# Kernel tuning notes

Measured on AMD Instinct MI355X. Metric: run time of the kernel, lower is better.

## Reference

```python
import jax, jax.numpy as jnp
import numpy as np

DIM = 2048
N_HEADS = 32
N_KV_HEADS = 8
HEAD_DIM = DIM // N_HEADS  # 64
SEQ = 2048
BATCH = 2


def _rope_freqs(seq_len, head_dim, theta=10000.0):
    inv = 1.0 / (theta ** (np.arange(0, head_dim, 2)[: head_dim // 2].astype(np.float32) / head_dim))
    t = np.arange(seq_len, dtype=np.float32)
    ang = np.outer(t, inv)  # (seq, head_dim//2)
    return jnp.asarray(np.cos(ang)), jnp.asarray(np.sin(ang))


def setup_inputs() -> dict:
    key = jax.random.key(0)
    ks = jax.random.split(key, 5)
    x = jax.random.normal(ks[0], (BATCH, SEQ, DIM), dtype=jnp.float32)
    s = 1.0 / np.sqrt(DIM)
    wq = jax.random.normal(ks[1], (N_HEADS * HEAD_DIM, DIM), dtype=jnp.float32) * s
    wk = jax.random.normal(ks[2], (N_KV_HEADS * HEAD_DIM, DIM), dtype=jnp.float32) * s
    wv = jax.random.normal(ks[3], (N_KV_HEADS * HEAD_DIM, DIM), dtype=jnp.float32) * s
    wo = jax.random.normal(ks[4], (DIM, N_HEADS * HEAD_DIM), dtype=jnp.float32) * s
    freqs_cos, freqs_sin = _rope_freqs(SEQ, HEAD_DIM)
    return {"x": x, "freqs_cos": freqs_cos, "freqs_sin": freqs_sin,
            "wq": wq, "wk": wk, "wv": wv, "wo": wo}


def _apply_rope(t, cos, sin):
    # t: (B, S, H, D); cos/sin: (S, D//2) broadcast to (1, S, 1, D//2)
    B, S, H, D = t.shape
    tr = t.reshape(B, S, H, D // 2, 2)
    x0, x1 = tr[..., 0], tr[..., 1]
    c = cos[None, :, None, :]
    s = sin[None, :, None, :]
    o0 = x0 * c - x1 * s
    o1 = x0 * s + x1 * c
    return jnp.stack([o0, o1], axis=-1).reshape(B, S, H, D)


def reference(x, freqs_cos, freqs_sin, wq, wk, wv, wo):
    B, S, _ = x.shape
    H, KV, D = N_HEADS, N_KV_HEADS, HEAD_DIM
    rep = H // KV
    xq = jnp.einsum('bsd,hd->bsh', x, wq).reshape(B, S, H, D)
    xk = jnp.einsum('bsd,hd->bsh', x, wk).reshape(B, S, KV, D)
    xv = jnp.einsum('bsd,hd->bsh', x, wv).reshape(B, S, KV, D)
    xq = _apply_rope(xq, freqs_cos, freqs_sin)
    xk = _apply_rope(xk, freqs_cos, freqs_sin)
    # GQA without materializing repeated K/V: group q heads as (KV, rep).
    # repeat_interleave on dim=2 maps q head h -> kv head h // rep.
    xqg = xq.reshape(B, S, KV, rep, D)
    scale = 1.0 / jnp.sqrt(jnp.float32(D))
    scores = jnp.einsum('bqkrd,bskd->bkrqs', xqg, xk) * scale  # (B,KV,rep,S,S)
    causal = jnp.tril(jnp.ones((S, S), dtype=bool))
    scores = jnp.where(causal[None, None, None], scores, jnp.float32(-jnp.inf))
    probs = jax.nn.softmax(scores, axis=-1)
    out = jnp.einsum('bkrqs,bskd->bqkrd', probs, xv)  # (B,S,KV,rep,D)
    out = out.reshape(B, S, H * D)
    return jnp.einsum('bsh,dh->bsd', out, wo)
```

## Files before the change

kernel.cpp:

```cpp
#include <hip/hip_runtime.h>

#define DIMSZ 2048
#define NH 32
#define NKV 8
#define HD 64
#define SEQLEN 2048
#define BATCH 2
#define NROWS (BATCH*SEQLEN)
#define NQKVC 3072

typedef __bf16 bf16x8 __attribute__((ext_vector_type(8)));
typedef __bf16 bf16x2 __attribute__((ext_vector_type(2)));
typedef float f32x4v __attribute__((ext_vector_type(4)));
typedef float f32x2v __attribute__((ext_vector_type(2)));
typedef float f32x16 __attribute__((ext_vector_type(16)));

__device__ __forceinline__ unsigned short f2bf(float f) {
  __bf16 h = (__bf16)f;
  union { __bf16 h; unsigned short u; } v; v.h = h; return v.u;
}
__device__ __forceinline__ unsigned int pk2bf(float lo, float hi) {
  f32x2v v; v[0] = lo; v[1] = hi;
  bf16x2 h = __builtin_convertvector(v, bf16x2);
  union { bf16x2 h; unsigned int u; } c; c.h = h; return c.u;
}
__device__ __forceinline__ int swz128(int row, int colBytes) {
  return row * 128 + (colBytes ^ ((row & 7) << 4));
}

#define GLOAD16(g, l) __builtin_amdgcn_global_load_lds( \
    (const __attribute__((address_space(1))) unsigned int*)(g), \
    (__attribute__((address_space(3))) unsigned int*)(l), 16, 0, 0)

__global__ void k_cvt_all(const float* __restrict__ x,
                          const float* __restrict__ wq, const float* __restrict__ wk,
                          const float* __restrict__ wv, const float* __restrict__ wo,
                          unsigned short* __restrict__ xb,
                          unsigned short* __restrict__ wqkvb,
                          unsigned short* __restrict__ wob) {
  int i = blockIdx.x * 256 + threadIdx.x;
  const float* s; unsigned short* d; int soff, doff;
  if (i < 2097152)        { s = x;  d = xb;    soff = i;           doff = i; }
  else if (i < 3145728)   { s = wq; d = wqkvb; soff = i - 2097152; doff = i - 2097152; }
  else if (i < 3407872)   { s = wk; d = wqkvb; soff = i - 3145728; doff = i - 2097152; }
  else if (i < 3670016)   { s = wv; d = wqkvb; soff = i - 3407872; doff = i - 2097152; }
  else                    { s = wo; d = wob;   soff = i - 3670016; doff = i - 3670016; }
  float4 v = reinterpret_cast<const float4*>(s)[soff];
  uint2 pk; pk.x = pk2bf(v.x, v.y); pk.y = pk2bf(v.z, v.w);
  reinterpret_cast<uint2*>(d)[doff] = pk;
}

__global__ __launch_bounds__(256, 2) void k_gemm_qkv(
    const unsigned short* __restrict__ A,
    const unsigned short* __restrict__ B,
    const float* __restrict__ fc, const float* __restrict__ fs,
    unsigned short* __restrict__ Qb, unsigned short* __restrict__ Kb,
    unsigned short* __restrict__ Vt)
{
  constexpr int BK = 64, K = DIMSZ;
  __shared__ __attribute__((aligned(16))) unsigned short smA[128 * BK];
  __shared__ __attribute__((aligned(16))) unsigned short smB[128 * BK];
  const int tid = threadIdx.x;
  const int lane = tid & 63;
  const int wid = tid >> 6;
  const int lr = lane & 15, lg = lane >> 4;
  const int gx = gridDim.x;
  int lin = blockIdx.y * gx + blockIdx.x;
  const int cpx = (gx * gridDim.y) >> 3;
  lin = (lin & 7) * cpx + (lin >> 3);
  const int m0 = (lin / gx) * 128, n0 = (lin % gx) * 128;
  const int wr = (wid >> 1) * 64, wc = (wid & 1) * 64;

  f32x4v acc[4][4];
  #pragma unroll
  for (int i = 0; i < 4; i++)
    #pragma unroll
    for (int j = 0; j < 4; j++)
      acc[i][j] = f32x4v{0.f, 0.f, 0.f, 0.f};

  for (int k0 = 0; k0 < K; k0 += BK) {
    #pragma unroll
    for (int c = 0; c < 4; c++) {
      const int chunk = wid * 4 + c;
      const int idx = chunk * 64 + lane;
      const int row = idx >> 3, s = idx & 7;
      const int ks = (s ^ (row & 7)) * 8;
      GLOAD16(A + (size_t)(m0 + row) * K + k0 + ks, &smA[chunk * 512]);
      GLOAD16(B + (size_t)(n0 + row) * K + k0 + ks, &smB[chunk * 512]);
    }
    __syncthreads();
    #pragma unroll
    for (int ks = 0; ks < 2; ks++) {
      bf16x8 af[4], bfv[4];
      #pragma unroll
      for (int m = 0; m < 4; m++)
        af[m] = *reinterpret_cast<const bf16x8*>((char*)smA + swz128(wr + m * 16 + lr, ks * 64 + lg * 16));
      #pragma unroll
      for (int n = 0; n < 4; n++)
        bfv[n] = *reinterpret_cast<const bf16x8*>((char*)smB + swz128(wc + n * 16 + lr, ks * 64 + lg * 16));
      #pragma unroll
      for (int m = 0; m < 4; m++)
        #pragma unroll
        for (int n = 0; n < 4; n++)
          acc[m][n] = __builtin_amdgcn_mfma_f32_16x16x32_bf16(af[m], bfv[n], acc[m][n], 0, 0, 0);
    }
    __syncthreads();
  }
  const int bx = n0 >> 7;
  if (bx < 20) {
    const bool isQ = bx < 16;
    const float SCL = isQ ? 0.18033688011112043f : 1.0f;
    #pragma unroll
    for (int n = 0; n < 4; n++) {
      const int col = n0 + wc + n * 16 + lr;
      const int d = col & 63;
      const int i = d >> 1;
      const float sgn = (d & 1) ? 1.0f : -1.0f;
      unsigned short* dst;
      if (isQ) dst = Qb + (size_t)(col >> 6) * (SEQLEN * HD) + d;
      else     dst = Kb + (size_t)((col - 2048) >> 6) * (SEQLEN * HD) + d;
      #pragma unroll
      for (int m = 0; m < 4; m++)
        #pragma unroll
        for (int r = 0; r < 4; r++) {
          const int row = m0 + wr + m * 16 + lg * 4 + r;
          const int s = row & (SEQLEN - 1), b = row >> 11;
          const float v = acc[m][n][r];
          const float p = __shfl_xor(v, 1);
          const float c = fc[s * 32 + i], sn = fs[s * 32 + i];
          const float o = (v * c + sgn * p * sn) * SCL;
          const size_t headStride = (size_t)(isQ ? NH : NKV) * SEQLEN * HD;
          dst[(size_t)b * headStride + (size_t)s * HD] = f2bf(o);
        }
    }
  } else {
    #pragma unroll
    for (int n = 0; n < 4; n++) {
      const int col = n0 + wc + n * 16 + lr;
      const int kvh = (col - 2560) >> 6, d = col & 63;
      #pragma unroll
      for (int m = 0; m < 4; m++) {
        const int row0 = m0 + wr + m * 16 + lg * 4;
        const int s0 = row0 & (SEQLEN - 1), b = row0 >> 11;
        uint2 pk;
        pk.x = pk2bf(acc[m][n][0], acc[m][n][1]);
        pk.y = pk2bf(acc[m][n][2], acc[m][n][3]);
        *reinterpret_cast<uint2*>(
            Vt + ((size_t)((b * NKV + kvh) * HD) + d) * SEQLEN + s0) = pk;
      }
    }
  }
}

template<int OUT_BF16>
__global__ __launch_bounds__(256, 2) void k_gemm_bt(
    const unsigned short* __restrict__ A,
    const unsigned short* __restrict__ B,
    void* __restrict__ Cv, int M, int N, int K)
{
  constexpr int BK = 64;
  __shared__ __attribute__((aligned(16))) unsigned short smA[128 * BK];
  __shared__ __attribute__((aligned(16))) unsigned short smB[128 * BK];
  const int tid = threadIdx.x;
  const int lane = tid & 63;
  const int wid = tid >> 6;
  const int lr = lane & 15, lg = lane >> 4;
  const int gx = gridDim.x;
  int lin = blockIdx.y * gx + blockIdx.x;
  const int cpx = (gx * gridDim.y) >> 3;
  lin = (lin & 7) * cpx + (lin >> 3);
  const int m0 = (lin / gx) * 128, n0 = (lin % gx) * 128;
  const int wr = (wid >> 1) * 64, wc = (wid & 1) * 64;

  f32x4v acc[4][4];
  #pragma unroll
  for (int i = 0; i < 4; i++)
    #pragma unroll
    for (int j = 0; j < 4; j++)
      acc[i][j] = f32x4v{0.f, 0.f, 0.f, 0.f};

  for (int k0 = 0; k0 < K; k0 += BK) {
    #pragma unroll
    for (int c = 0; c < 4; c++) {
      const int chunk = wid * 4 + c;
      const int idx = chunk * 64 + lane;
      const int row = idx >> 3, s = idx & 7;
      const int ks = (s ^ (row & 7)) * 8;
      GLOAD16(A + (size_t)(m0 + row) * K + k0 + ks, &smA[chunk * 512]);
      GLOAD16(B + (size_t)(n0 + row) * K + k0 + ks, &smB[chunk * 512]);
    }
    __syncthreads();
    #pragma unroll
    for (int ks = 0; ks < 2; ks++) {
      bf16x8 af[4], bfv[4];
      #pragma unroll
      for (int m = 0; m < 4; m++)
        af[m] = *reinterpret_cast<const bf16x8*>((char*)smA + swz128(wr + m * 16 + lr, ks * 64 + lg * 16));
      #pragma unroll
      for (int n = 0; n < 4; n++)
        bfv[n] = *reinterpret_cast<const bf16x8*>((char*)smB + swz128(wc + n * 16 + lr, ks * 64 + lg * 16));
      #pragma unroll
      for (int m = 0; m < 4; m++)
        #pragma unroll
        for (int n = 0; n < 4; n++)
          acc[m][n] = __builtin_amdgcn_mfma_f32_16x16x32_bf16(af[m], bfv[n], acc[m][n], 0, 0, 0);
    }
    __syncthreads();
  }
  #pragma unroll
  for (int m = 0; m < 4; m++)
    #pragma unroll
    for (int n = 0; n < 4; n++)
      #pragma unroll
      for (int r = 0; r < 4; r++) {
        const size_t row = m0 + wr + m * 16 + lg * 4 + r;
        const size_t col = n0 + wc + n * 16 + lr;
        if (OUT_BF16) ((unsigned short*)Cv)[row * N + col] = f2bf(acc[m][n][r]);
        else          ((float*)Cv)[row * N + col] = acc[m][n][r];
      }
}

__global__ __launch_bounds__(256, 2) void k_attn(
    const unsigned short* __restrict__ Qg,
    const unsigned short* __restrict__ Kg,
    const unsigned short* __restrict__ Vt,
    unsigned short* __restrict__ Og)
{
  constexpr int KVB = 64;
  __shared__ __attribute__((aligned(16))) unsigned short sK0[KVB * HD];
  __shared__ __attribute__((aligned(16))) unsigned short sK1[KVB * HD];
  __shared__ __attribute__((aligned(16))) unsigned short sV0[HD * KVB];
  __shared__ __attribute__((aligned(16))) unsigned short sV1[HD * KVB];
  const int tid = threadIdx.x;
  const int lane = tid & 63, wid = tid >> 6;
  const int l31 = lane & 31, hi = lane >> 5;
  const int g = blockIdx.x;
  const int i = g >> 3;
  const int r = i >> 5;
  const int c = i & 31;
  const int p = (g & 7) * 2 + (c >> 4);
  const int kvh = p & 7, b = p >> 3;
  const int h = kvh * 4 + r;
  const int s4 = c & 15;
  const int qt = (r & 1) ? s4 : 15 - s4;
  const unsigned short* Qp = Qg + ((size_t)(b * NH + h) * SEQLEN) * HD;
  const unsigned short* Kp = Kg + ((size_t)(b * NKV + kvh) * SEQLEN) * HD;
  const unsigned short* Vp = Vt + ((size_t)(b * NKV + kvh) * HD) * SEQLEN;

  int srow[2], scol[2];
  #pragma unroll
  for (int cc = 0; cc < 2; cc++) {
    const int idx = (wid * 2 + cc) * 64 + lane;
    srow[cc] = idx >> 3;
    scol[cc] = ((idx & 7) ^ (srow[cc] & 7)) * 8;
  }

  const int qrow0 = qt * 128 + wid * 32;
  const int qg = qrow0 + l31;
  bf16x8 aq[4];
  #pragma unroll
  for (int ks = 0; ks < 4; ks++)
    aq[ks] = *reinterpret_cast<const bf16x8*>(Qp + (size_t)qg * HD + ks * 16 + hi * 8);

  f32x16 accO0, accO1;
  #pragma unroll
  for (int ii = 0; ii < 16; ii++) { accO0[ii] = 0.f; accO1[ii] = 0.f; }
  float mrun = -3.0e38f, lrun = 0.f;

  auto compute = [&](int kv0, auto& sKb, auto& sVb) {
    if (kv0 > qrow0 + 31) return;
    f32x16 S0, S1;
    #pragma unroll
    for (int ii = 0; ii < 16; ii++) { S0[ii] = 0.f; S1[ii] = 0.f; }
    __builtin_amdgcn_s_setprio(1);
    #pragma unroll
    for (int ks = 0; ks < 4; ks++) {
      bf16x8 ak0 = *reinterpret_cast<const bf16x8*>((char*)sKb + swz128(l31,      ks * 32 + hi * 16));
      bf16x8 ak1 = *reinterpret_cast<const bf16x8*>((char*)sKb + swz128(32 + l31, ks * 32 + hi * 16));
      S0 = __builtin_amdgcn_mfma_f32_32x32x16_bf16(ak0, aq[ks], S0, 0, 0, 0);
      S1 = __builtin_amdgcn_mfma_f32_32x32x16_bf16(ak1, aq[ks], S1, 0, 0, 0);
    }
    __builtin_amdgcn_s_setprio(0);
    if (kv0 + KVB - 1 > qrow0) {
      #pragma unroll
      for (int reg = 0; reg < 16; reg++) {
        const int rl = (reg & 3) + 8 * (reg >> 2) + (hi << 2);
        if (kv0 + rl > qg)      S0[reg] = -1.0e30f;
        if (kv0 + 32 + rl > qg) S1[reg] = -1.0e30f;
      }
    }
    float t16[16];
    #pragma unroll
    for (int ii = 0; ii < 16; ii++) t16[ii] = fmaxf(S0[ii], S1[ii]);
    float t8[8];
    #pragma unroll
    for (int ii = 0; ii < 8; ii++) t8[ii] = fmaxf(t16[ii], t16[ii + 8]);
    float t4[4];
    #pragma unroll
    for (int ii = 0; ii < 4; ii++) t4[ii] = fmaxf(t8[ii], t8[ii + 4]);
    float tm = fmaxf(fmaxf(t4[0], t4[1]), fmaxf(t4[2], t4[3]));
    tm = fmaxf(tm, __shfl_xor(tm, 32));
    const float mo = mrun;
    const bool defer = __all(tm <= mo + 8.0f);
    const float mn = defer ? mo : fmaxf(mo, tm);
    #pragma unroll
    for (int ii = 0; ii < 16; ii++) {
      S0[ii] = __builtin_amdgcn_exp2f(S0[ii] - mn);
      S1[ii] = __builtin_amdgcn_exp2f(S1[ii] - mn);
    }
    float u16[16];
    #pragma unroll
    for (int ii = 0; ii < 16; ii++) u16[ii] = S0[ii] + S1[ii];
    float u8[8];
    #pragma unroll
    for (int ii = 0; ii < 8; ii++) u8[ii] = u16[ii] + u16[ii + 8];
    float u4[4];
    #pragma unroll
    for (int ii = 0; ii < 4; ii++) u4[ii] = u8[ii] + u8[ii + 4];
    float rs = (u4[0] + u4[1]) + (u4[2] + u4[3]);
    rs += __shfl_xor(rs, 32);
    if (defer) {
      lrun += rs;
    } else {
      const float sc = __builtin_amdgcn_exp2f(mo - mn);
      mrun = mn;
      lrun = lrun * sc + rs;
      #pragma unroll
      for (int reg = 0; reg < 16; reg++) {
        const int rl = (reg & 3) + 8 * (reg >> 2) + (hi << 2);
        const float scr = __shfl(sc, rl);
        accO0[reg] *= scr; accO1[reg] *= scr;
      }
    }
    __builtin_amdgcn_s_setprio(1);
    #define PVSTEP(S16, G, CB) do {                                          \
      unsigned a0 = pk2bf(S16[(G)+0], S16[(G)+1]);                           \
      unsigned a1 = pk2bf(S16[(G)+2], S16[(G)+3]);                           \
      unsigned b0 = pk2bf(S16[(G)+4], S16[(G)+5]);                           \
      unsigned b1 = pk2bf(S16[(G)+6], S16[(G)+7]);                           \
      unsigned s0 = hi ? a0 : b0, s1 = hi ? a1 : b1;                         \
      unsigned r0 = __shfl_xor((int)s0, 32), r1 = __shfl_xor((int)s1, 32);   \
      union { unsigned u[4]; bf16x8 v; } pf;                                 \
      pf.u[0] = hi ? r0 : a0; pf.u[1] = hi ? r1 : a1;                        \
      pf.u[2] = hi ? b0 : r0; pf.u[3] = hi ? b1 : r1;                        \
      bf16x8 bv0 = *reinterpret_cast<const bf16x8*>((char*)sVb + swz128(l31,      (CB))); \
      bf16x8 bv1 = *reinterpret_cast<const bf16x8*>((char*)sVb + swz128(32 + l31, (CB))); \
      accO0 = __builtin_amdgcn_mfma_f32_32x32x16_bf16(pf.v, bv0, accO0, 0, 0, 0); \
      accO1 = __builtin_amdgcn_mfma_f32_32x32x16_bf16(pf.v, bv1, accO1, 0, 0, 0); \
    } while (0)
    PVSTEP(S0, 0,  0  + hi * 16);
    PVSTEP(S0, 8,  32 + hi * 16);
    PVSTEP(S1, 0,  64 + hi * 16);
    PVSTEP(S1, 8,  96 + hi * 16);
    #undef PVSTEP
    __builtin_amdgcn_s_setprio(0);
  };

  const int nt = qt * 2 + 2;
  GLOAD16(Kp + (size_t)srow[0] * HD + scol[0], &sK0[(wid * 2 + 0) * 512]);
  GLOAD16(Kp + (size_t)srow[1] * HD + scol[1], &sK0[(wid * 2 + 1) * 512]);
  GLOAD16(Vp + (size_t)srow[0] * SEQLEN + scol[0], &sV0[(wid * 2 + 0) * 512]);
  GLOAD16(Vp + (size_t)srow[1] * SEQLEN + scol[1], &sV0[(wid * 2 + 1) * 512]);
  __syncthreads();
  for (int t = 0; t < nt; t += 2) {
    {
      const int kn = (t + 1) * KVB;
      GLOAD16(Kp + (size_t)(kn + srow[0]) * HD + scol[0], &sK1[(wid * 2 + 0) * 512]);
      GLOAD16(Kp + (size_t)(kn + srow[1]) * HD + scol[1], &sK1[(wid * 2 + 1) * 512]);
      GLOAD16(Vp + (size_t)srow[0] * SEQLEN + kn + scol[0], &sV1[(wid * 2 + 0) * 512]);
      GLOAD16(Vp + (size_t)srow[1] * SEQLEN + kn + scol[1], &sV1[(wid * 2 + 1) * 512]);
    }
    compute(t * KVB, sK0, sV0);
    __syncthreads();
    if (t + 2 < nt) {
      const int kn = (t + 2) * KVB;
      GLOAD16(Kp + (size_t)(kn + srow[0]) * HD + scol[0], &sK0[(wid * 2 + 0) * 512]);
      GLOAD16(Kp + (size_t)(kn + srow[1]) * HD + scol[1], &sK0[(wid * 2 + 1) * 512]);
      GLOAD16(Vp + (size_t)srow[0] * SEQLEN + kn + scol[0], &sV0[(wid * 2 + 0) * 512]);
      GLOAD16(Vp + (size_t)srow[1] * SEQLEN + kn + scol[1], &sV0[(wid * 2 + 1) * 512]);
    }
    compute((t + 1) * KVB, sK1, sV1);
    __syncthreads();
  }
  const float inv = 1.0f / lrun;
  #pragma unroll
  for (int reg = 0; reg < 16; reg++) {
    const int rl = (reg & 3) + 8 * (reg >> 2) + (hi << 2);
    const float invr = __shfl(inv, rl);
    const int q = qrow0 + rl;
    const size_t base = ((size_t)(b * SEQLEN + q)) * DIMSZ + h * HD;
    Og[base + l31]      = f2bf(accO0[reg] * invr);
    Og[base + 32 + l31] = f2bf(accO1[reg] * invr);
  }
}

extern "C" void kernel_launch(void* const* d_in, const int* in_sizes, int n_in,
                              void* d_out, int out_size, void* d_ws, size_t ws_size,
                              hipStream_t stream)
{
  const float* x  = (const float*)d_in[0];
  const float* fc = (const float*)d_in[1];
  const float* fs = (const float*)d_in[2];
  const float* wq = (const float*)d_in[3];
  const float* wk = (const float*)d_in[4];
  const float* wv = (const float*)d_in[5];
  const float* wo = (const float*)d_in[6];
  float* out = (float*)d_out;
  char* ws = (char*)d_ws;

  unsigned short* xb    = (unsigned short*)(ws + 0);
  unsigned short* wqkvb = (unsigned short*)(ws + 16777216);
  unsigned short* wob   = (unsigned short*)(ws + 29360128);
  unsigned short* Qb    = (unsigned short*)(ws + 62914560);
  unsigned short* Kb    = (unsigned short*)(ws + 79691776);
  unsigned short* Vtb   = (unsigned short*)(ws + 83886080);
  unsigned short* attnb = (unsigned short*)(ws + 88080384);

  k_cvt_all<<<18432, 256, 0, stream>>>(x, wq, wk, wv, wo, xb, wqkvb, wob);

  dim3 g1(24, 32);
  k_gemm_qkv<<<g1, 256, 0, stream>>>(xb, wqkvb, fc, fs, Qb, Kb, Vtb);

  k_attn<<<1024, 256, 0, stream>>>(Qb, Kb, Vtb, attnb);

  dim3 g2(16, 32);
  k_gemm_bt<0><<<g2, 256, 0, stream>>>(attnb, wob, out, NROWS, DIMSZ, DIMSZ);
}
```

Measured before the change: 188.9 us.

## Double attention query tile to 256 rows with 8 waves per block

The attention kernel now launches 512 blocks of 512 threads, each covering 256 query rows (8 waves of 32 rows) instead of 128 rows with 4 waves. Each K/V tile loaded into shared memory is reused by twice as many query rows, and each thread issues one cooperative load instead of two, which cuts global/L2 traffic per query row. Block scheduling changes from an interleaved/mirrored qt order to a longest-first descending order. In exchange, fewer and larger blocks may worsen load balance across the causal triangle, early waves idle on fully masked tiles, and launch_bounds(512,2) tightens the register budget.

```diff
diff --git a/kernel.cpp b/kernel.cpp
--- a/kernel.cpp
+++ b/kernel.cpp
@@ -220,7 +220,7 @@
       }
 }
 
-__global__ __launch_bounds__(256, 2) void k_attn(
+__global__ __launch_bounds__(512, 2) void k_attn(
     const unsigned short* __restrict__ Qg,
     const unsigned short* __restrict__ Kg,
     const unsigned short* __restrict__ Vt,
@@ -235,27 +235,21 @@
   const int lane = tid & 63, wid = tid >> 6;
   const int l31 = lane & 31, hi = lane >> 5;
   const int g = blockIdx.x;
-  const int i = g >> 3;
-  const int r = i >> 5;
-  const int c = i & 31;
-  const int p = (g & 7) * 2 + (c >> 4);
+  const int c = g >> 3;
+  const int qt = 7 - (c >> 3);
+  const int rem = c & 7;
+  const int p = (g & 7) * 2 + (rem >> 2);
   const int kvh = p & 7, b = p >> 3;
-  const int h = kvh * 4 + r;
-  const int s4 = c & 15;
-  const int qt = (r & 1) ? s4 : 15 - s4;
+  const int h = kvh * 4 + (rem & 3);
   const unsigned short* Qp = Qg + ((size_t)(b * NH + h) * SEQLEN) * HD;
   const unsigned short* Kp = Kg + ((size_t)(b * NKV + kvh) * SEQLEN) * HD;
   const unsigned short* Vp = Vt + ((size_t)(b * NKV + kvh) * HD) * SEQLEN;
 
-  int srow[2], scol[2];
-  #pragma unroll
-  for (int cc = 0; cc < 2; cc++) {
-    const int idx = (wid * 2 + cc) * 64 + lane;
-    srow[cc] = idx >> 3;
-    scol[cc] = ((idx & 7) ^ (srow[cc] & 7)) * 8;
-  }
-
-  const int qrow0 = qt * 128 + wid * 32;
+  const int sidx = wid * 64 + lane;
+  const int srow = sidx >> 3;
+  const int scol = ((sidx & 7) ^ (srow & 7)) * 8;
+
+  const int qrow0 = qt * 256 + wid * 32;
   const int qg = qrow0 + l31;
   bf16x8 aq[4];
   #pragma unroll
@@ -356,28 +350,22 @@
     __builtin_amdgcn_s_setprio(0);
   };
 
-  const int nt = qt * 2 + 2;
-  GLOAD16(Kp + (size_t)srow[0] * HD + scol[0], &sK0[(wid * 2 + 0) * 512]);
-  GLOAD16(Kp + (size_t)srow[1] * HD + scol[1], &sK0[(wid * 2 + 1) * 512]);
-  GLOAD16(Vp + (size_t)srow[0] * SEQLEN + scol[0], &sV0[(wid * 2 + 0) * 512]);
-  GLOAD16(Vp + (size_t)srow[1] * SEQLEN + scol[1], &sV0[(wid * 2 + 1) * 512]);
+  const int nt = (qt + 1) * 4;
+  GLOAD16(Kp + (size_t)srow * HD + scol, &sK0[wid * 512]);
+  GLOAD16(Vp + (size_t)srow * SEQLEN + scol, &sV0[wid * 512]);
   __syncthreads();
   for (int t = 0; t < nt; t += 2) {
     {
       const int kn = (t + 1) * KVB;
-      GLOAD16(Kp + (size_t)(kn + srow[0]) * HD + scol[0], &sK1[(wid * 2 + 0) * 512]);
-      GLOAD16(Kp + (size_t)(kn + srow[1]) * HD + scol[1], &sK1[(wid * 2 + 1) * 512]);
-      GLOAD16(Vp + (size_t)srow[0] * SEQLEN + kn + scol[0], &sV1[(wid * 2 + 0) * 512]);
-      GLOAD16(Vp + (size_t)srow[1] * SEQLEN + kn + scol[1], &sV1[(wid * 2 + 1) * 512]);
+      GLOAD16(Kp + (size_t)(kn + srow) * HD + scol, &sK1[wid * 512]);
+      GLOAD16(Vp + (size_t)srow * SEQLEN + kn + scol, &sV1[wid * 512]);
     }
     compute(t * KVB, sK0, sV0);
     __syncthreads();
     if (t + 2 < nt) {
       const int kn = (t + 2) * KVB;
-      GLOAD16(Kp + (size_t)(kn + srow[0]) * HD + scol[0], &sK0[(wid * 2 + 0) * 512]);
-      GLOAD16(Kp + (size_t)(kn + srow[1]) * HD + scol[1], &sK0[(wid * 2 + 1) * 512]);
-      GLOAD16(Vp + (size_t)srow[0] * SEQLEN + kn + scol[0], &sV0[(wid * 2 + 0) * 512]);
-      GLOAD16(Vp + (size_t)srow[1] * SEQLEN + kn + scol[1], &sV0[(wid * 2 + 1) * 512]);
+      GLOAD16(Kp + (size_t)(kn + srow) * HD + scol, &sK0[wid * 512]);
+      GLOAD16(Vp + (size_t)srow * SEQLEN + kn + scol, &sV0[wid * 512]);
     }
     compute((t + 1) * KVB, sK1, sV1);
     __syncthreads();
@@ -421,7 +409,7 @@
   dim3 g1(24, 32);
   k_gemm_qkv<<<g1, 256, 0, stream>>>(xb, wqkvb, fc, fs, Qb, Kb, Vtb);
 
-  k_attn<<<1024, 256, 0, stream>>>(Qb, Kb, Vtb, attnb);
+  k_attn<<<512, 512, 0, stream>>>(Qb, Kb, Vtb, attnb);
 
   dim3 g2(16, 32);
   k_gemm_bt<0><<<g2, 256, 0, stream>>>(attnb, wob, out, NROWS, DIMSZ, DIMSZ);
```

After: 171.6 us. 9.2% less time.

## Pair causal q-tiles per block and software-pipeline QK with softmax-PV

Applied to the files above, without the earlier changes.

Each attention block now handles two query tiles (qp and 15-qp), so every block does the same amount of causal work, and the grid is halved to 512. Inside the KV loop, K and V are staged separately, and the QK^T MFMAs for the next tile are issued before the softmax and PV of the current tile. The aim is to overlap matrix-core work with the exp and reduction work and to remove tail imbalance. This holds two sets of score registers at once, which raises register pressure and may cut occupancy, and the smaller grid leaves fewer blocks to hide latency.

```diff
diff --git a/kernel.cpp b/kernel.cpp
--- a/kernel.cpp
+++ b/kernel.cpp
@@ -234,15 +234,12 @@
   const int tid = threadIdx.x;
   const int lane = tid & 63, wid = tid >> 6;
   const int l31 = lane & 31, hi = lane >> 5;
-  const int g = blockIdx.x;
-  const int i = g >> 3;
-  const int r = i >> 5;
-  const int c = i & 31;
-  const int p = (g & 7) * 2 + (c >> 4);
-  const int kvh = p & 7, b = p >> 3;
-  const int h = kvh * 4 + r;
-  const int s4 = c & 15;
-  const int qt = (r & 1) ? s4 : 15 - s4;
+  const int orig = blockIdx.x;
+  const int w = (orig & 7) * 64 + (orig >> 3);
+  const int kvh = w >> 6;
+  const int b = (w >> 5) & 1;
+  const int h = kvh * 4 + ((w >> 3) & 3);
+  const int qp = w & 7;
   const unsigned short* Qp = Qg + ((size_t)(b * NH + h) * SEQLEN) * HD;
   const unsigned short* Kp = Kg + ((size_t)(b * NKV + kvh) * SEQLEN) * HD;
   const unsigned short* Vp = Vt + ((size_t)(b * NKV + kvh) * HD) * SEQLEN;
@@ -255,142 +252,149 @@
     scol[cc] = ((idx & 7) ^ (srow[cc] & 7)) * 8;
   }
 
-  const int qrow0 = qt * 128 + wid * 32;
-  const int qg = qrow0 + l31;
-  bf16x8 aq[4];
-  #pragma unroll
-  for (int ks = 0; ks < 4; ks++)
-    aq[ks] = *reinterpret_cast<const bf16x8*>(Qp + (size_t)qg * HD + ks * 16 + hi * 8);
-
-  f32x16 accO0, accO1;
-  #pragma unroll
-  for (int ii = 0; ii < 16; ii++) { accO0[ii] = 0.f; accO1[ii] = 0.f; }
-  float mrun = -3.0e38f, lrun = 0.f;
-
-  auto compute = [&](int kv0, auto& sKb, auto& sVb) {
-    if (kv0 > qrow0 + 31) return;
-    f32x16 S0, S1;
-    #pragma unroll
-    for (int ii = 0; ii < 16; ii++) { S0[ii] = 0.f; S1[ii] = 0.f; }
-    __builtin_amdgcn_s_setprio(1);
-    #pragma unroll
-    for (int ks = 0; ks < 4; ks++) {
-      bf16x8 ak0 = *reinterpret_cast<const bf16x8*>((char*)sKb + swz128(l31,      ks * 32 + hi * 16));
-      bf16x8 ak1 = *reinterpret_cast<const bf16x8*>((char*)sKb + swz128(32 + l31, ks * 32 + hi * 16));
-      S0 = __builtin_amdgcn_mfma_f32_32x32x16_bf16(ak0, aq[ks], S0, 0, 0, 0);
-      S1 = __builtin_amdgcn_mfma_f32_32x32x16_bf16(ak1, aq[ks], S1, 0, 0, 0);
-    }
-    __builtin_amdgcn_s_setprio(0);
-    if (kv0 + KVB - 1 > qrow0) {
-      #pragma unroll
-      for (int reg = 0; reg < 16; reg++) {
-        const int rl = (reg & 3) + 8 * (reg >> 2) + (hi << 2);
-        if (kv0 + rl > qg)      S0[reg] = -1.0e30f;
-        if (kv0 + 32 + rl > qg) S1[reg] = -1.0e30f;
-      }
-    }
-    float t16[16];
-    #pragma unroll
-    for (int ii = 0; ii < 16; ii++) t16[ii] = fmaxf(S0[ii], S1[ii]);
-    float t8[8];
-    #pragma unroll
-    for (int ii = 0; ii < 8; ii++) t8[ii] = fmaxf(t16[ii], t16[ii + 8]);
-    float t4[4];
-    #pragma unroll
-    for (int ii = 0; ii < 4; ii++) t4[ii] = fmaxf(t8[ii], t8[ii + 4]);
-    float tm = fmaxf(fmaxf(t4[0], t4[1]), fmaxf(t4[2], t4[3]));
-    tm = fmaxf(tm, __shfl_xor(tm, 32));
-    const float mo = mrun;
-    const bool defer = __all(tm <= mo + 8.0f);
-    const float mn = defer ? mo : fmaxf(mo, tm);
-    #pragma unroll
-    for (int ii = 0; ii < 16; ii++) {
-      S0[ii] = __builtin_amdgcn_exp2f(S0[ii] - mn);
-      S1[ii] = __builtin_amdgcn_exp2f(S1[ii] - mn);
-    }
-    float u16[16];
-    #pragma unroll
-    for (int ii = 0; ii < 16; ii++) u16[ii] = S0[ii] + S1[ii];
-    float u8[8];
-    #pragma unroll
-    for (int ii = 0; ii < 8; ii++) u8[ii] = u16[ii] + u16[ii + 8];
-    float u4[4];
-    #pragma unroll
-    for (int ii = 0; ii < 4; ii++) u4[ii] = u8[ii] + u8[ii + 4];
-    float rs = (u4[0] + u4[1]) + (u4[2] + u4[3]);
-    rs += __shfl_xor(rs, 32);
-    if (defer) {
-      lrun += rs;
-    } else {
-      const float sc = __builtin_amdgcn_exp2f(mo - mn);
-      mrun = mn;
-      lrun = lrun * sc + rs;
-      #pragma unroll
-      for (int reg = 0; reg < 16; reg++) {
-        const int rl = (reg & 3) + 8 * (reg >> 2) + (hi << 2);
-        const float scr = __shfl(sc, rl);
-        accO0[reg] *= scr; accO1[reg] *= scr;
-      }
-    }
-    __builtin_amdgcn_s_setprio(1);
-    #define PVSTEP(S16, G, CB) do {                                          \
-      unsigned a0 = pk2bf(S16[(G)+0], S16[(G)+1]);                           \
-      unsigned a1 = pk2bf(S16[(G)+2], S16[(G)+3]);                           \
-      unsigned b0 = pk2bf(S16[(G)+4], S16[(G)+5]);                           \
-      unsigned b1 = pk2bf(S16[(G)+6], S16[(G)+7]);                           \
-      unsigned s0 = hi ? a0 : b0, s1 = hi ? a1 : b1;                         \
-      unsigned r0 = __shfl_xor((int)s0, 32), r1 = __shfl_xor((int)s1, 32);   \
-      union { unsigned u[4]; bf16x8 v; } pf;                                 \
-      pf.u[0] = hi ? r0 : a0; pf.u[1] = hi ? r1 : a1;                        \
-      pf.u[2] = hi ? b0 : r0; pf.u[3] = hi ? b1 : r1;                        \
-      bf16x8 bv0 = *reinterpret_cast<const bf16x8*>((char*)sVb + swz128(l31,      (CB))); \
-      bf16x8 bv1 = *reinterpret_cast<const bf16x8*>((char*)sVb + swz128(32 + l31, (CB))); \
-      accO0 = __builtin_amdgcn_mfma_f32_32x32x16_bf16(pf.v, bv0, accO0, 0, 0, 0); \
-      accO1 = __builtin_amdgcn_mfma_f32_32x32x16_bf16(pf.v, bv1, accO1, 0, 0, 0); \
-    } while (0)
-    PVSTEP(S0, 0,  0  + hi * 16);
-    PVSTEP(S0, 8,  32 + hi * 16);
-    PVSTEP(S1, 0,  64 + hi * 16);
-    PVSTEP(S1, 8,  96 + hi * 16);
-    #undef PVSTEP
-    __builtin_amdgcn_s_setprio(0);
-  };
-
-  const int nt = qt * 2 + 2;
-  GLOAD16(Kp + (size_t)srow[0] * HD + scol[0], &sK0[(wid * 2 + 0) * 512]);
-  GLOAD16(Kp + (size_t)srow[1] * HD + scol[1], &sK0[(wid * 2 + 1) * 512]);
-  GLOAD16(Vp + (size_t)srow[0] * SEQLEN + scol[0], &sV0[(wid * 2 + 0) * 512]);
-  GLOAD16(Vp + (size_t)srow[1] * SEQLEN + scol[1], &sV0[(wid * 2 + 1) * 512]);
-  __syncthreads();
-  for (int t = 0; t < nt; t += 2) {
-    {
-      const int kn = (t + 1) * KVB;
-      GLOAD16(Kp + (size_t)(kn + srow[0]) * HD + scol[0], &sK1[(wid * 2 + 0) * 512]);
-      GLOAD16(Kp + (size_t)(kn + srow[1]) * HD + scol[1], &sK1[(wid * 2 + 1) * 512]);
-      GLOAD16(Vp + (size_t)srow[0] * SEQLEN + kn + scol[0], &sV1[(wid * 2 + 0) * 512]);
-      GLOAD16(Vp + (size_t)srow[1] * SEQLEN + kn + scol[1], &sV1[(wid * 2 + 1) * 512]);
-    }
-    compute(t * KVB, sK0, sV0);
+  for (int phase = 0; phase < 2; phase++) {
+    const int qt = phase ? (15 - qp) : qp;
+    const int qrow0 = qt * 128 + wid * 32;
+    const int qg = qrow0 + l31;
+    bf16x8 aq[4];
+    #pragma unroll
+    for (int ks = 0; ks < 4; ks++)
+      aq[ks] = *reinterpret_cast<const bf16x8*>(Qp + (size_t)qg * HD + ks * 16 + hi * 8);
+
+    f32x16 accO0, accO1;
+    #pragma unroll
+    for (int ii = 0; ii < 16; ii++) { accO0[ii] = 0.f; accO1[ii] = 0.f; }
+    float mrun = -3.0e38f, lrun = 0.f;
+
+    auto STAGE_K = [&](int t, unsigned short* buf) {
+      #pragma unroll
+      for (int cc = 0; cc < 2; cc++)
+        GLOAD16(Kp + (size_t)(t * KVB + srow[cc]) * HD + scol[cc], &buf[(wid * 2 + cc) * 512]);
+    };
+    auto STAGE_V = [&](int t, unsigned short* buf) {
+      #pragma unroll
+      for (int cc = 0; cc < 2; cc++)
+        GLOAD16(Vp + (size_t)srow[cc] * SEQLEN + t * KVB + scol[cc], &buf[(wid * 2 + cc) * 512]);
+    };
+    auto QK = [&](int kv0, const unsigned short* bK, f32x16& S0, f32x16& S1) {
+      if (kv0 > qrow0 + 31) return;
+      #pragma unroll
+      for (int ii = 0; ii < 16; ii++) { S0[ii] = 0.f; S1[ii] = 0.f; }
+      __builtin_amdgcn_s_setprio(1);
+      #pragma unroll
+      for (int ks = 0; ks < 4; ks++) {
+        bf16x8 ak0 = *reinterpret_cast<const bf16x8*>((const char*)bK + swz128(l31,      ks * 32 + hi * 16));
+        bf16x8 ak1 = *reinterpret_cast<const bf16x8*>((const char*)bK + swz128(32 + l31, ks * 32 + hi * 16));
+        S0 = __builtin_amdgcn_mfma_f32_32x32x16_bf16(ak0, aq[ks], S0, 0, 0, 0);
+        S1 = __builtin_amdgcn_mfma_f32_32x32x16_bf16(ak1, aq[ks], S1, 0, 0, 0);
+      }
+      __builtin_amdgcn_s_setprio(0);
+    };
+    auto SMPV = [&](int kv0, const unsigned short* bV, f32x16& S0, f32x16& S1) {
+      if (kv0 > qrow0 + 31) return;
+      if (kv0 + KVB - 1 > qrow0) {
+        #pragma unroll
+        for (int reg = 0; reg < 16; reg++) {
+          const int rl = (reg & 3) + 8 * (reg >> 2) + (hi << 2);
+          if (kv0 + rl > qg)      S0[reg] = -1.0e30f;
+          if (kv0 + 32 + rl > qg) S1[reg] = -1.0e30f;
+        }
+      }
+      float t16[16];
+      #pragma unroll
+      for (int ii = 0; ii < 16; ii++) t16[ii] = fmaxf(S0[ii], S1[ii]);
+      float t8[8];
+      #pragma unroll
+      for (int ii = 0; ii < 8; ii++) t8[ii] = fmaxf(t16[ii], t16[ii + 8]);
+      float t4[4];
+      #pragma unroll
+      for (int ii = 0; ii < 4; ii++) t4[ii] = fmaxf(t8[ii], t8[ii + 4]);
+      float tm = fmaxf(fmaxf(t4[0], t4[1]), fmaxf(t4[2], t4[3]));
+      tm = fmaxf(tm, __shfl_xor(tm, 32));
+      const float mo = mrun;
+      const bool defer = __all(tm <= mo + 8.0f);
+      const float mn = defer ? mo : fmaxf(mo, tm);
+      #pragma unroll
+      for (int ii = 0; ii < 16; ii++) {
+        S0[ii] = __builtin_amdgcn_exp2f(S0[ii] - mn);
+        S1[ii] = __builtin_amdgcn_exp2f(S1[ii] - mn);
+      }
+      float u16[16];
+      #pragma unroll
+      for (int ii = 0; ii < 16; ii++) u16[ii] = S0[ii] + S1[ii];
+      float u8[8];
+      #pragma unroll
+      for (int ii = 0; ii < 8; ii++) u8[ii] = u16[ii] + u16[ii + 8];
+      float u4[4];
+      #pragma unroll
+      for (int ii = 0; ii < 4; ii++) u4[ii] = u8[ii] + u8[ii + 4];
+      float rs = (u4[0] + u4[1]) + (u4[2] + u4[3]);
+      rs += __shfl_xor(rs, 32);
+      if (defer) {
+        lrun += rs;
+      } else {
+        const float sc = __builtin_amdgcn_exp2f(mo - mn);
+        mrun = mn;
+        lrun = lrun * sc + rs;
+        #pragma unroll
+        for (int reg = 0; reg < 16; reg++) {
+          const int rl = (reg & 3) + 8 * (reg >> 2) + (hi << 2);
+          const float scr = __shfl(sc, rl);
+          accO0[reg] *= scr; accO1[reg] *= scr;
+        }
+      }
+      __builtin_amdgcn_s_setprio(1);
+      #define PVSTEP(S16, G, CB) do {                                          \
+        unsigned a0 = pk2bf(S16[(G)+0], S16[(G)+1]);                           \
+        unsigned a1 = pk2bf(S16[(G)+2], S16[(G)+3]);                           \
+        unsigned b0 = pk2bf(S16[(G)+4], S16[(G)+5]);                           \
+        unsigned b1 = pk2bf(S16[(G)+6], S16[(G)+7]);                           \
+        unsigned s0 = hi ? a0 : b0, s1 = hi ? a1 : b1;                         \
+        unsigned r0 = __shfl_xor((int)s0, 32), r1 = __shfl_xor((int)s1, 32);   \
+        union { unsigned u[4]; bf16x8 v; } pf;                                 \
+        pf.u[0] = hi ? r0 : a0; pf.u[1] = hi ? r1 : a1;                        \
+        pf.u[2] = hi ? b0 : r0; pf.u[3] = hi ? b1 : r1;                        \
+        bf16x8 bv0 = *reinterpret_cast<const bf16x8*>((const char*)bV + swz128(l31,      (CB))); \
+        bf16x8 bv1 = *reinterpret_cast<const bf16x8*>((const char*)bV + swz128(32 + l31, (CB))); \
+        accO0 = __builtin_amdgcn_mfma_f32_32x32x16_bf16(pf.v, bv0, accO0, 0, 0, 0); \
+        accO1 = __builtin_amdgcn_mfma_f32_32x32x16_bf16(pf.v, bv1, accO1, 0, 0, 0); \
+      } while (0)
+      PVSTEP(S0, 0,  0  + hi * 16);
+      PVSTEP(S0, 8,  32 + hi * 16);
+      PVSTEP(S1, 0,  64 + hi * 16);
+      PVSTEP(S1, 8,  96 + hi * 16);
+      #undef PVSTEP
+      __builtin_amdgcn_s_setprio(0);
+    };
+
+    const int nt = qt * 2 + 2;
+    f32x16 Sa0, Sa1, Sb0, Sb1;
+    STAGE_K(0, sK0);
+    STAGE_V(0, sV0);
     __syncthreads();
-    if (t + 2 < nt) {
-      const int kn = (t + 2) * KVB;
-      GLOAD16(Kp + (size_t)(kn + srow[0]) * HD + scol[0], &sK0[(wid * 2 + 0) * 512]);
-      GLOAD16(Kp + (size_t)(kn + srow[1]) * HD + scol[1], &sK0[(wid * 2 + 1) * 512]);
-      GLOAD16(Vp + (size_t)srow[0] * SEQLEN + kn + scol[0], &sV0[(wid * 2 + 0) * 512]);
-      GLOAD16(Vp + (size_t)srow[1] * SEQLEN + kn + scol[1], &sV0[(wid * 2 + 1) * 512]);
-    }
-    compute((t + 1) * KVB, sK1, sV1);
-    __syncthreads();
-  }
-  const float inv = 1.0f / lrun;
-  #pragma unroll
-  for (int reg = 0; reg < 16; reg++) {
-    const int rl = (reg & 3) + 8 * (reg >> 2) + (hi << 2);
-    const float invr = __shfl(inv, rl);
-    const int q = qrow0 + rl;
-    const size_t base = ((size_t)(b * SEQLEN + q)) * DIMSZ + h * HD;
-    Og[base + l31]      = f2bf(accO0[reg] * invr);
-    Og[base + 32 + l31] = f2bf(accO1[reg] * invr);
+    STAGE_K(1, sK1);
+    QK(0, sK0, Sa0, Sa1);
+    for (int t = 0; t < nt; t += 2) {
+      __syncthreads();
+      if (t + 2 < nt) STAGE_K(t + 2, sK0);
+      STAGE_V(t + 1, sV1);
+      QK((t + 1) * KVB, sK1, Sb0, Sb1);
+      SMPV(t * KVB, sV0, Sa0, Sa1);
+      __syncthreads();
+      if (t + 3 < nt) STAGE_K(t + 3, sK1);
+      if (t + 2 < nt) { STAGE_V(t + 2, sV0); QK((t + 2) * KVB, sK0, Sa0, Sa1); }
+      SMPV((t + 1) * KVB, sV1, Sb0, Sb1);
+    }
+    const float inv = 1.0f / lrun;
+    #pragma unroll
+    for (int reg = 0; reg < 16; reg++) {
+      const int rl = (reg & 3) + 8 * (reg >> 2) + (hi << 2);
+      const float invr = __shfl(inv, rl);
+      const int q = qrow0 + rl;
+      const size_t base = ((size_t)(b * SEQLEN + q)) * DIMSZ + h * HD;
+      Og[base + l31]      = f2bf(accO0[reg] * invr);
+      Og[base + 32 + l31] = f2bf(accO1[reg] * invr);
+    }
   }
 }
 
@@ -421,7 +425,7 @@
   dim3 g1(24, 32);
   k_gemm_qkv<<<g1, 256, 0, stream>>>(xb, wqkvb, fc, fs, Qb, Kb, Vtb);
 
-  k_attn<<<1024, 256, 0, stream>>>(Qb, Kb, Vtb, attnb);
+  k_attn<<<512, 256, 0, stream>>>(Qb, Kb, Vtb, attnb);
 
   dim3 g2(16, 32);
   k_gemm_bt<0><<<g2, 256, 0, stream>>>(attnb, wob, out, NROWS, DIMSZ, DIMSZ);
```

New measurement: 171.4 us. 1.1x faster.

## Pair causal q-tiles per attention block to balance work across 512 blocks

Applied to the files above, without the earlier changes.

Each attention block now handles two query tiles, qp and 15-qp, one after the other, so every block does the same total causal work. The grid shrinks from 1024 to 512 blocks and the block-to-head mapping is remapped with an XCD-style interleave. This targets load imbalance and tail effects from uneven causal tile sizes. In exchange each block runs serially longer and there are fewer blocks to hide latency, and K/V tiles are reloaded for the second phase.

```diff
diff --git a/kernel.cpp b/kernel.cpp
--- a/kernel.cpp
+++ b/kernel.cpp
@@ -234,15 +234,12 @@
   const int tid = threadIdx.x;
   const int lane = tid & 63, wid = tid >> 6;
   const int l31 = lane & 31, hi = lane >> 5;
-  const int g = blockIdx.x;
-  const int i = g >> 3;
-  const int r = i >> 5;
-  const int c = i & 31;
-  const int p = (g & 7) * 2 + (c >> 4);
-  const int kvh = p & 7, b = p >> 3;
-  const int h = kvh * 4 + r;
-  const int s4 = c & 15;
-  const int qt = (r & 1) ? s4 : 15 - s4;
+  const int orig = blockIdx.x;
+  const int w = (orig & 7) * 64 + (orig >> 3);
+  const int kvh = w >> 6;
+  const int b = (w >> 5) & 1;
+  const int h = kvh * 4 + ((w >> 3) & 3);
+  const int qp = w & 7;
   const unsigned short* Qp = Qg + ((size_t)(b * NH + h) * SEQLEN) * HD;
   const unsigned short* Kp = Kg + ((size_t)(b * NKV + kvh) * SEQLEN) * HD;
   const unsigned short* Vp = Vt + ((size_t)(b * NKV + kvh) * HD) * SEQLEN;
@@ -255,142 +252,137 @@
     scol[cc] = ((idx & 7) ^ (srow[cc] & 7)) * 8;
   }
 
-  const int qrow0 = qt * 128 + wid * 32;
-  const int qg = qrow0 + l31;
-  bf16x8 aq[4];
-  #pragma unroll
-  for (int ks = 0; ks < 4; ks++)
-    aq[ks] = *reinterpret_cast<const bf16x8*>(Qp + (size_t)qg * HD + ks * 16 + hi * 8);
-
-  f32x16 accO0, accO1;
-  #pragma unroll
-  for (int ii = 0; ii < 16; ii++) { accO0[ii] = 0.f; accO1[ii] = 0.f; }
-  float mrun = -3.0e38f, lrun = 0.f;
-
-  auto compute = [&](int kv0, auto& sKb, auto& sVb) {
-    if (kv0 > qrow0 + 31) return;
-    f32x16 S0, S1;
-    #pragma unroll
-    for (int ii = 0; ii < 16; ii++) { S0[ii] = 0.f; S1[ii] = 0.f; }
-    __builtin_amdgcn_s_setprio(1);
-    #pragma unroll
-    for (int ks = 0; ks < 4; ks++) {
-      bf16x8 ak0 = *reinterpret_cast<const bf16x8*>((char*)sKb + swz128(l31,      ks * 32 + hi * 16));
-      bf16x8 ak1 = *reinterpret_cast<const bf16x8*>((char*)sKb + swz128(32 + l31, ks * 32 + hi * 16));
-      S0 = __builtin_amdgcn_mfma_f32_32x32x16_bf16(ak0, aq[ks], S0, 0, 0, 0);
-      S1 = __builtin_amdgcn_mfma_f32_32x32x16_bf16(ak1, aq[ks], S1, 0, 0, 0);
-    }
-    __builtin_amdgcn_s_setprio(0);
-    if (kv0 + KVB - 1 > qrow0) {
-      #pragma unroll
-      for (int reg = 0; reg < 16; reg++) {
-        const int rl = (reg & 3) + 8 * (reg >> 2) + (hi << 2);
-        if (kv0 + rl > qg)      S0[reg] = -1.0e30f;
-        if (kv0 + 32 + rl > qg) S1[reg] = -1.0e30f;
-      }
-    }
-    float t16[16];
-    #pragma unroll
-    for (int ii = 0; ii < 16; ii++) t16[ii] = fmaxf(S0[ii], S1[ii]);
-    float t8[8];
-    #pragma unroll
-    for (int ii = 0; ii < 8; ii++) t8[ii] = fmaxf(t16[ii], t16[ii + 8]);
-    float t4[4];
-    #pragma unroll
-    for (int ii = 0; ii < 4; ii++) t4[ii] = fmaxf(t8[ii], t8[ii + 4]);
-    float tm = fmaxf(fmaxf(t4[0], t4[1]), fmaxf(t4[2], t4[3]));
-    tm = fmaxf(tm, __shfl_xor(tm, 32));
-    const float mo = mrun;
-    const bool defer = __all(tm <= mo + 8.0f);
-    const float mn = defer ? mo : fmaxf(mo, tm);
-    #pragma unroll
-    for (int ii = 0; ii < 16; ii++) {
-      S0[ii] = __builtin_amdgcn_exp2f(S0[ii] - mn);
-      S1[ii] = __builtin_amdgcn_exp2f(S1[ii] - mn);
-    }
-    float u16[16];
-    #pragma unroll
-    for (int ii = 0; ii < 16; ii++) u16[ii] = S0[ii] + S1[ii];
-    float u8[8];
-    #pragma unroll
-    for (int ii = 0; ii < 8; ii++) u8[ii] = u16[ii] + u16[ii + 8];
-    float u4[4];
-    #pragma unroll
-    for (int ii = 0; ii < 4; ii++) u4[ii] = u8[ii] + u8[ii + 4];
-    float rs = (u4[0] + u4[1]) + (u4[2] + u4[3]);
-    rs += __shfl_xor(rs, 32);
-    if (defer) {
-      lrun += rs;
-    } else {
-      const float sc = __builtin_amdgcn_exp2f(mo - mn);
-      mrun = mn;
-      lrun = lrun * sc + rs;
-      #pragma unroll
-      for (int reg = 0; reg < 16; reg++) {
-        const int rl = (reg & 3) + 8 * (reg >> 2) + (hi << 2);
-        const float scr = __shfl(sc, rl);
-        accO0[reg] *= scr; accO1[reg] *= scr;
-      }
-    }
-    __builtin_amdgcn_s_setprio(1);
-    #define PVSTEP(S16, G, CB) do {                                          \
-      unsigned a0 = pk2bf(S16[(G)+0], S16[(G)+1]);                           \
-      unsigned a1 = pk2bf(S16[(G)+2], S16[(G)+3]);                           \
-      unsigned b0 = pk2bf(S16[(G)+4], S16[(G)+5]);                           \
-      unsigned b1 = pk2bf(S16[(G)+6], S16[(G)+7]);                           \
-      unsigned s0 = hi ? a0 : b0, s1 = hi ? a1 : b1;                         \
-      unsigned r0 = __shfl_xor((int)s0, 32), r1 = __shfl_xor((int)s1, 32);   \
-      union { unsigned u[4]; bf16x8 v; } pf;                                 \
-      pf.u[0] = hi ? r0 : a0; pf.u[1] = hi ? r1 : a1;                        \
-      pf.u[2] = hi ? b0 : r0; pf.u[3] = hi ? b1 : r1;                        \
-      bf16x8 bv0 = *reinterpret_cast<const bf16x8*>((char*)sVb + swz128(l31,      (CB))); \
-      bf16x8 bv1 = *reinterpret_cast<const bf16x8*>((char*)sVb + swz128(32 + l31, (CB))); \
-      accO0 = __builtin_amdgcn_mfma_f32_32x32x16_bf16(pf.v, bv0, accO0, 0, 0, 0); \
-      accO1 = __builtin_amdgcn_mfma_f32_32x32x16_bf16(pf.v, bv1, accO1, 0, 0, 0); \
+  for (int phase = 0; phase < 2; phase++) {
+    const int qt = phase ? (15 - qp) : qp;
+    const int qrow0 = qt * 128 + wid * 32;
+    const int qg = qrow0 + l31;
+    bf16x8 aq[4];
+    #pragma unroll
+    for (int ks = 0; ks < 4; ks++)
+      aq[ks] = *reinterpret_cast<const bf16x8*>(Qp + (size_t)qg * HD + ks * 16 + hi * 8);
+
+    f32x16 accO0, accO1;
+    #pragma unroll
+    for (int ii = 0; ii < 16; ii++) { accO0[ii] = 0.f; accO1[ii] = 0.f; }
+    float mrun = -3.0e38f, lrun = 0.f;
+
+    auto compute = [&](int kv0, auto& sKb, auto& sVb) {
+      if (kv0 > qrow0 + 31) return;
+      f32x16 S0, S1;
+      #pragma unroll
+      for (int ii = 0; ii < 16; ii++) { S0[ii] = 0.f; S1[ii] = 0.f; }
+      __builtin_amdgcn_s_setprio(1);
+      #pragma unroll
+      for (int ks = 0; ks < 4; ks++) {
+        bf16x8 ak0 = *reinterpret_cast<const bf16x8*>((char*)sKb + swz128(l31,      ks * 32 + hi * 16));
+        bf16x8 ak1 = *reinterpret_cast<const bf16x8*>((char*)sKb + swz128(32 + l31, ks * 32 + hi * 16));
+        S0 = __builtin_amdgcn_mfma_f32_32x32x16_bf16(ak0, aq[ks], S0, 0, 0, 0);
+        S1 = __builtin_amdgcn_mfma_f32_32x32x16_bf16(ak1, aq[ks], S1, 0, 0, 0);
+      }
+      __builtin_amdgcn_s_setprio(0);
+      if (kv0 + KVB - 1 > qrow0) {
+        #pragma unroll
+        for (int reg = 0; reg < 16; reg++) {
+          const int rl = (reg & 3) + 8 * (reg >> 2) + (hi << 2);
+          if (kv0 + rl > qg)      S0[reg] = -1.0e30f;
+          if (kv0 + 32 + rl > qg) S1[reg] = -1.0e30f;
+        }
+      }
+      float t16[16];
+      #pragma unroll
+      for (int ii = 0; ii < 16; ii++) t16[ii] = fmaxf(S0[ii], S1[ii]);
+      float t8[8];
+      #pragma unroll
+      for (int ii = 0; ii < 8; ii++) t8[ii] = fmaxf(t16[ii], t16[ii + 8]);
+      float t4[4];
+      #pragma unroll
+      for (int ii = 0; ii < 4; ii++) t4[ii] = fmaxf(t8[ii], t8[ii + 4]);
+      float tm = fmaxf(fmaxf(t4[0], t4[1]), fmaxf(t4[2], t4[3]));
+      tm = fmaxf(tm, __shfl_xor(tm, 32));
+      const float mo = mrun;
+      const bool defer = __all(tm <= mo + 8.0f);
+      const float mn = defer ? mo : fmaxf(mo, tm);
+      #pragma unroll
+      for (int ii = 0; ii < 16; ii++) {
+        S0[ii] = __builtin_amdgcn_exp2f(S0[ii] - mn);
+        S1[ii] = __builtin_amdgcn_exp2f(S1[ii] - mn);
+      }
+      float u16[16];
+      #pragma unroll
+      for (int ii = 0; ii < 16; ii++) u16[ii] = S0[ii] + S1[ii];
+      float u8[8];
+      #pragma unroll
+      for (int ii = 0; ii < 8; ii++) u8[ii] = u16[ii] + u16[ii + 8];
+      float u4[4];
+      #pragma unroll
+      for (int ii = 0; ii < 4; ii++) u4[ii] = u8[ii] + u8[ii + 4];
+      float rs = (u4[0] + u4[1]) + (u4[2] + u4[3]);
+      rs += __shfl_xor(rs, 32);
+      if (defer) {
+        lrun += rs;
+      } else {
+        const float sc = __builtin_amdgcn_exp2f(mo - mn);
+        mrun = mn;
+        lrun = lrun * sc + rs;
+        #pragma unroll
+        for (int reg = 0; reg < 16; reg++) {
+          const int rl = (reg & 3) + 8 * (reg >> 2) + (hi << 2);
+          const float scr = __shfl(sc, rl);
+          accO0[reg] *= scr; accO1[reg] *= scr;
+        }
+      }
+      __builtin_amdgcn_s_setprio(1);
+      #define PVSTEP(S16, G, CB) do {                                          \
+        unsigned a0 = pk2bf(S16[(G)+0], S16[(G)+1]);                           \
+        unsigned a1 = pk2bf(S16[(G)+2], S16[(G)+3]);                           \
+        unsigned b0 = pk2bf(S16[(G)+4], S16[(G)+5]);                           \
+        unsigned b1 = pk2bf(S16[(G)+6], S16[(G)+7]);                           \
+        unsigned s0 = hi ? a0 : b0, s1 = hi ? a1 : b1;                         \
+        unsigned r0 = __shfl_xor((int)s0, 32), r1 = __shfl_xor((int)s1, 32);   \
+        union { unsigned u[4]; bf16x8 v; } pf;                                 \
+        pf.u[0] = hi ? r0 : a0; pf.u[1] = hi ? r1 : a1;                        \
+        pf.u[2] = hi ? b0 : r0; pf.u[3] = hi ? b1 : r1;                        \
+        bf16x8 bv0 = *reinterpret_cast<const bf16x8*>((char*)sVb + swz128(l31,      (CB))); \
+        bf16x8 bv1 = *reinterpret_cast<const bf16x8*>((char*)sVb + swz128(32 + l31, (CB))); \
+        accO0 = __builtin_amdgcn_mfma_f32_32x32x16_bf16(pf.v, bv0, accO0, 0, 0, 0); \
+        accO1 = __builtin_amdgcn_mfma_f32_32x32x16_bf16(pf.v, bv1, accO1, 0, 0, 0); \
+      } while (0)
+      PVSTEP(S0, 0,  0  + hi * 16);
+      PVSTEP(S0, 8,  32 + hi * 16);
+      PVSTEP(S1, 0,  64 + hi * 16);
+      PVSTEP(S1, 8,  96 + hi * 16);
+      #undef PVSTEP
+      __builtin_amdgcn_s_setprio(0);
+    };
+
+    const int nt = qt * 2 + 2;
+    #define STAGE_PAIR(t, bufK, bufV) do {                                     \
+      GLOAD16(Kp + (size_t)((t) * KVB + srow[0]) * HD + scol[0], &bufK[(wid * 2 + 0) * 512]); \
+      GLOAD16(Kp + (size_t)((t) * KVB + srow[1]) * HD + scol[1], &bufK[(wid * 2 + 1) * 512]); \
+      GLOAD16(Vp + (size_t)srow[0] * SEQLEN + (t) * KVB + scol[0], &bufV[(wid * 2 + 0) * 512]); \
+      GLOAD16(Vp + (size_t)srow[1] * SEQLEN + (t) * KVB + scol[1], &bufV[(wid * 2 + 1) * 512]); \
     } while (0)
-    PVSTEP(S0, 0,  0  + hi * 16);
-    PVSTEP(S0, 8,  32 + hi * 16);
-    PVSTEP(S1, 0,  64 + hi * 16);
-    PVSTEP(S1, 8,  96 + hi * 16);
-    #undef PVSTEP
-    __builtin_amdgcn_s_setprio(0);
-  };
-
-  const int nt = qt * 2 + 2;
-  GLOAD16(Kp + (size_t)srow[0] * HD + scol[0], &sK0[(wid * 2 + 0) * 512]);
-  GLOAD16(Kp + (size_t)srow[1] * HD + scol[1], &sK0[(wid * 2 + 1) * 512]);
-  GLOAD16(Vp + (size_t)srow[0] * SEQLEN + scol[0], &sV0[(wid * 2 + 0) * 512]);
-  GLOAD16(Vp + (size_t)srow[1] * SEQLEN + scol[1], &sV0[(wid * 2 + 1) * 512]);
-  __syncthreads();
-  for (int t = 0; t < nt; t += 2) {
-    {
-      const int kn = (t + 1) * KVB;
-      GLOAD16(Kp + (size_t)(kn + srow[0]) * HD + scol[0], &sK1[(wid * 2 + 0) * 512]);
-      GLOAD16(Kp + (size_t)(kn + srow[1]) * HD + scol[1], &sK1[(wid * 2 + 1) * 512]);
-      GLOAD16(Vp + (size_t)srow[0] * SEQLEN + kn + scol[0], &sV1[(wid * 2 + 0) * 512]);
-      GLOAD16(Vp + (size_t)srow[1] * SEQLEN + kn + scol[1], &sV1[(wid * 2 + 1) * 512]);
-    }
-    compute(t * KVB, sK0, sV0);
+    STAGE_PAIR(0, sK0, sV0);
     __syncthreads();
-    if (t + 2 < nt) {
-      const int kn = (t + 2) * KVB;
-      GLOAD16(Kp + (size_t)(kn + srow[0]) * HD + scol[0], &sK0[(wid * 2 + 0) * 512]);
-      GLOAD16(Kp + (size_t)(kn + srow[1]) * HD + scol[1], &sK0[(wid * 2 + 1) * 512]);
-      GLOAD16(Vp + (size_t)srow[0] * SEQLEN + kn + scol[0], &sV0[(wid * 2 + 0) * 512]);
-      GLOAD16(Vp + (size_t)srow[1] * SEQLEN + kn + scol[1], &sV0[(wid * 2 + 1) * 512]);
-    }
-    compute((t + 1) * KVB, sK1, sV1);
-    __syncthreads();
-  }
-  const float inv = 1.0f / lrun;
-  #pragma unroll
-  for (int reg = 0; reg < 16; reg++) {
-    const int rl = (reg & 3) + 8 * (reg >> 2) + (hi << 2);
-    const float invr = __shfl(inv, rl);
-    const int q = qrow0 + rl;
-    const size_t base = ((size_t)(b * SEQLEN + q)) * DIMSZ + h * HD;
-    Og[base + l31]      = f2bf(accO0[reg] * invr);
-    Og[base + 32 + l31] = f2bf(accO1[reg] * invr);
+    for (int t = 0; t < nt; t += 2) {
+      STAGE_PAIR(t + 1, sK1, sV1);
+      compute(t * KVB, sK0, sV0);
+      __syncthreads();
+      if (t + 2 < nt) STAGE_PAIR(t + 2, sK0, sV0);
+      compute((t + 1) * KVB, sK1, sV1);
+      __syncthreads();
+    }
+    #undef STAGE_PAIR
+    const float inv = 1.0f / lrun;
+    #pragma unroll
+    for (int reg = 0; reg < 16; reg++) {
+      const int rl = (reg & 3) + 8 * (reg >> 2) + (hi << 2);
+      const float invr = __shfl(inv, rl);
+      const int q = qrow0 + rl;
+      const size_t base = ((size_t)(b * SEQLEN + q)) * DIMSZ + h * HD;
+      Og[base + l31]      = f2bf(accO0[reg] * invr);
+      Og[base + 32 + l31] = f2bf(accO1[reg] * invr);
+    }
   }
 }
 
@@ -421,7 +413,7 @@
   dim3 g1(24, 32);
   k_gemm_qkv<<<g1, 256, 0, stream>>>(xb, wqkvb, fc, fs, Qb, Kb, Vtb);
 
-  k_attn<<<1024, 256, 0, stream>>>(Qb, Kb, Vtb, attnb);
+  k_attn<<<512, 256, 0, stream>>>(Qb, Kb, Vtb, attnb);
 
   dim3 g2(16, 32);
   k_gemm_bt<0><<<g2, 256, 0, stream>>>(attnb, wob, out, NROWS, DIMSZ, DIMSZ);
```

After: 173.1 us. 1.09x faster.
